# Kernel tuning notes

Measured on AMD Instinct MI355X. Metric: run time of the kernel, lower is better.

Reference implementation:

```python
import jax, jax.numpy as jnp
import numpy as np
import math

SEQ_LEN = 2048
EMB = 1024
HEAD = 64
BATCH = 8

def setup_inputs() -> dict:
    key = jax.random.key(0)
    k1, k2, k3, k4 = jax.random.split(key, 4)
    x = jax.random.normal(k1, (BATCH, SEQ_LEN, EMB), dtype=jnp.float32)
    # torch Linear(no bias): out = x @ W.T with W [out,in]; store as [in,out]
    s = 1.0 / math.sqrt(EMB)
    Wk = jax.random.uniform(k2, (EMB, HEAD), dtype=jnp.float32, minval=-s, maxval=s)
    Wq = jax.random.uniform(k3, (EMB, HEAD), dtype=jnp.float32, minval=-s, maxval=s)
    Wv = jax.random.uniform(k4, (EMB, HEAD), dtype=jnp.float32, minval=-s, maxval=s)
    return {"x": x, "Wk": Wk, "Wq": Wq, "Wv": Wv}

def reference(x, Wk, Wq, Wv):
    B, S, E = x.shape
    H = Wk.shape[1]
    k = x @ Wk  # [B,S,H]
    q = x @ Wq
    v = x @ Wv
    scores = jnp.einsum('bsh,bth->bst', q, k) / math.sqrt(H)
    causal = jnp.tril(jnp.ones((S, S), dtype=bool))
    scores = jnp.where(causal[None], scores, -jnp.inf)
    attn = jax.nn.softmax(scores, axis=-1)
    # dropout is identity in eval mode
    return jnp.einsum('bst,bth->bsh', attn, v)
```

## Files before the change

### kernel.cpp

```cpp
#include <hip/hip_runtime.h>
#include <hip/hip_bf16.h>

typedef __attribute__((ext_vector_type(8))) short short8;
typedef __attribute__((ext_vector_type(4))) short short4v;
typedef __attribute__((ext_vector_type(4))) float floatx4;

#define SEQ   2048
#define EMB   1024
#define HEAD  64
#define BATCH 8

__device__ __forceinline__ short f2bf(float f) {
    union { float f; unsigned u; } a; a.f = f;
    unsigned u = a.u;
    u = (u + 0x7FFFu + ((u >> 16) & 1u)) >> 16;
    return (short)u;
}

__device__ __forceinline__ void gld16(const void* g, void* l) {
    __builtin_amdgcn_global_load_lds(
        (const __attribute__((address_space(1))) unsigned int*)g,
        (__attribute__((address_space(3))) unsigned int*)l,
        16, 0, 0);
}

__global__ void wtrans_kernel(const float* __restrict__ Wk,
                              const float* __restrict__ Wq,
                              const float* __restrict__ Wv,
                              short* __restrict__ Wf) {
    int gid  = blockIdx.x * 256 + threadIdx.x;
    int lane = gid & 63;
    int fid  = gid >> 6;
    int chunk = fid & 31;
    int mnt  = fid >> 5;
    int mat  = mnt >> 2, nt = mnt & 3;
    const float* src = (mat == 0) ? Wq : (mat == 1) ? Wk : Wv;
    int n = lane & 15, quad = lane >> 4;
    int h = nt * 16 + n;
    short8 o8;
    #pragma unroll
    for (int j = 0; j < 8; ++j)
        o8[j] = f2bf(src[(chunk * 32 + quad * 8 + j) * 64 + h]);
    *(short8*)(Wf + (long)gid * 8) = o8;
}

__global__ __launch_bounds__(256, 1) void qkv_kernel(const float* __restrict__ x,
                                                     const short* __restrict__ Wf,
                                                     short* __restrict__ q,
                                                     short* __restrict__ k,
                                                     short* __restrict__ vt) {
    __shared__ short LW[2][12][4][64][8];
    const int wv   = threadIdx.x >> 6;
    const int lane = threadIdx.x & 63;
    const int l15  = lane & 15;
    const int quad = lane >> 4;
    const int row0 = blockIdx.x * 64 + wv * 16;

    floatx4 acc[12];
    #pragma unroll
    for (int f = 0; f < 12; ++f) acc[f] = (floatx4){0.f, 0.f, 0.f, 0.f};

    const float* xrow = x + (long)(row0 + l15) * EMB + quad * 8;

    #pragma unroll
    for (int i = 0; i < 12; ++i) {
        const int s = wv * 12 + i, mnt = s >> 2, c = s & 3;
        gld16(Wf + (long)(mnt * 32 + c) * 512 + lane * 8, &LW[0][mnt][c][0][0]);
    }
    __syncthreads();

    #pragma unroll 1
    for (int g = 0; g < 8; ++g) {
        const int bb = g & 1;
        const float* xg = xrow + g * 128;
        floatx4 xv[8];
        #pragma unroll
        for (int c = 0; c < 4; ++c) {
            xv[2 * c]     = *(const floatx4*)(xg + c * 32);
            xv[2 * c + 1] = *(const floatx4*)(xg + c * 32 + 4);
        }
        if (g < 7) {
            #pragma unroll
            for (int i = 0; i < 12; ++i) {
                const int s = wv * 12 + i, mnt = s >> 2, c = s & 3;
                gld16(Wf + (long)(mnt * 32 + (g + 1) * 4 + c) * 512 + lane * 8,
                      &LW[bb ^ 1][mnt][c][0][0]);
            }
        }
        #pragma unroll
        for (int c = 0; c < 4; ++c) {
            short8 a;
            #pragma unroll
            for (int i = 0; i < 4; ++i) {
                a[i]     = f2bf(xv[2 * c][i]);
                a[4 + i] = f2bf(xv[2 * c + 1][i]);
            }
            #pragma unroll
            for (int f = 0; f < 12; ++f) {
                short8 bf = *(const short8*)&LW[bb][f][c][lane][0];
                acc[f] = __builtin_amdgcn_mfma_f32_16x16x32_bf16(a, bf, acc[f], 0, 0, 0);
            }
        }
        __syncthreads();
    }

    const int bidx = row0 >> 11;
    const int srow = (row0 & (SEQ - 1)) + quad * 4;
    #pragma unroll
    for (int nt = 0; nt < 4; ++nt) {
        const int col = nt * 16 + l15;
        #pragma unroll
        for (int r = 0; r < 4; ++r) {
            long grow = (long)(row0 + quad * 4 + r);
            q[grow * HEAD + col] = f2bf(acc[nt][r]);
            k[grow * HEAD + col] = f2bf(acc[4 + nt][r]);
        }
        short4v vv;
        #pragma unroll
        for (int r = 0; r < 4; ++r) vv[r] = f2bf(acc[8 + nt][r]);
        *(short4v*)(vt + ((long)bidx * HEAD + col) * SEQ + srow) = vv;
    }
}

__global__ __launch_bounds__(256, 2) void attn_kernel(const short* __restrict__ q,
                                                      const short* __restrict__ k,
                                                      const short* __restrict__ vt,
                                                      float* __restrict__ out) {
    __shared__ short KV[2][16][64][8];
    __shared__ short Plds[4][16][40];
    __shared__ float oT[2][2][16][64];
    __shared__ float lT[2][2][16];

    const int wv   = threadIdx.x >> 6;
    const int lane = threadIdx.x & 63;
    const int l15  = lane & 15;
    const int quad = lane >> 4;
    const int rg   = wv & 1;
    const int kh   = wv >> 1;
    const int b    = blockIdx.x & 7;
    const int p    = blockIdx.x >> 3;
    const int t2   = 63 - p;
    const int s1   = p * 32, s2 = t2 * 32;
    const int nch1 = (p >> 1) + 1;
    const int nch2 = (t2 >> 1) + 1;

    const short* kbase = k  + (long)b * SEQ * HEAD;
    const short* vbase = vt + (long)b * HEAD * SEQ;

    const short* q1p = q + ((long)b * SEQ + s1 + rg * 16 + l15) * HEAD + quad * 8;
    const short* q2p = q + ((long)b * SEQ + s2 + rg * 16 + l15) * HEAD + quad * 8;
    short8 q1f0 = *(const short8*)(q1p), q1f1 = *(const short8*)(q1p + 32);
    short8 q2f0 = *(const short8*)(q2p), q2f1 = *(const short8*)(q2p + 32);

    floatx4 o1[4], o2[4];
    #pragma unroll
    for (int nh = 0; nh < 4; ++nh) {
        o1[nh] = (floatx4){0.f, 0.f, 0.f, 0.f};
        o2[nh] = (floatx4){0.f, 0.f, 0.f, 0.f};
    }
    float l1[4] = {0.f, 0.f, 0.f, 0.f};
    float l2[4] = {0.f, 0.f, 0.f, 0.f};

    auto stage = [&](int ch, int bb) {
        const int j0 = ch * 64;
        #pragma unroll
        for (int i = 0; i < 2; ++i) {
            const int fid = wv + i * 4;
            const int ntg = fid >> 1, ks = fid & 1;
            gld16(kbase + (long)(j0 + ntg * 16 + l15) * HEAD + ks * 32 + quad * 8,
                  &KV[bb][fid][0][0]);
        }
        #pragma unroll
        for (int i = 0; i < 2; ++i) {
            const int fid = wv + i * 4;
            const int kh2 = fid >> 2, nth = fid & 3;
            gld16(vbase + (long)(nth * 16 + l15) * SEQ + j0 + kh2 * 32 + quad * 8,
                  &KV[bb][8 + fid][0][0]);
        }
    };

    stage(0, 0);
    __syncthreads();

    #pragma unroll 1
    for (int ch = 0; ch < nch2; ++ch) {
        const int bb = ch & 1;
        if (ch + 1 < nch2) stage(ch + 1, bb ^ 1);
        const int j0 = ch * 64;

        short8 kf[2][2], vf[4];
        #pragma unroll
        for (int nt = 0; nt < 2; ++nt)
            #pragma unroll
            for (int ks = 0; ks < 2; ++ks)
                kf[nt][ks] = *(const short8*)&KV[bb][(kh * 2 + nt) * 2 + ks][lane][0];
        #pragma unroll
        for (int nh = 0; nh < 4; ++nh)
            vf[nh] = *(const short8*)&KV[bb][8 + kh * 4 + nh][lane][0];

        {
            floatx4 sa[2];
            sa[0] = (floatx4){0.f, 0.f, 0.f, 0.f};
            sa[1] = (floatx4){0.f, 0.f, 0.f, 0.f};
            #pragma unroll
            for (int nt = 0; nt < 2; ++nt) {
                sa[nt] = __builtin_amdgcn_mfma_f32_16x16x32_bf16(q2f0, kf[nt][0], sa[nt], 0, 0, 0);
                sa[nt] = __builtin_amdgcn_mfma_f32_16x16x32_bf16(q2f1, kf[nt][1], sa[nt], 0, 0, 0);
            }
            #pragma unroll
            for (int r = 0; r < 4; ++r) {
                const int sq = s2 + rg * 16 + quad * 4 + r;
                #pragma unroll
                for (int nt = 0; nt < 2; ++nt) {
                    const int sk = j0 + kh * 32 + nt * 16 + l15;
                    float pv = (sk > sq) ? 0.f : __expf(sa[nt][r] * 0.125f - 16.f);
                    sa[nt][r] = pv;
                    l2[r] += pv;
                }
            }
            #pragma unroll
            for (int nt = 0; nt < 2; ++nt)
                #pragma unroll
                for (int r = 0; r < 4; ++r)
                    Plds[wv][quad * 4 + r][nt * 16 + l15] = f2bf(sa[nt][r]);
            short8 pf = *(const short8*)(&Plds[wv][l15][quad * 8]);
            #pragma unroll
            for (int nh = 0; nh < 4; ++nh)
                o2[nh] = __builtin_amdgcn_mfma_f32_16x16x32_bf16(pf, vf[nh], o2[nh], 0, 0, 0);
        }

        if (ch < nch1) {
            floatx4 sa[2];
            sa[0] = (floatx4){0.f, 0.f, 0.f, 0.f};
            sa[1] = (floatx4){0.f, 0.f, 0.f, 0.f};
            #pragma unroll
            for (int nt = 0; nt < 2; ++nt) {
                sa[nt] = __builtin_amdgcn_mfma_f32_16x16x32_bf16(q1f0, kf[nt][0], sa[nt], 0, 0, 0);
                sa[nt] = __builtin_amdgcn_mfma_f32_16x16x32_bf16(q1f1, kf[nt][1], sa[nt], 0, 0, 0);
            }
            #pragma unroll
            for (int r = 0; r < 4; ++r) {
                const int sq = s1 + rg * 16 + quad * 4 + r;
                #pragma unroll
                for (int nt = 0; nt < 2; ++nt) {
                    const int sk = j0 + kh * 32 + nt * 16 + l15;
                    float pv = (sk > sq) ? 0.f : __expf(sa[nt][r] * 0.125f - 16.f);
                    sa[nt][r] = pv;
                    l1[r] += pv;
                }
            }
            #pragma unroll
            for (int nt = 0; nt < 2; ++nt)
                #pragma unroll
                for (int r = 0; r < 4; ++r)
                    Plds[wv][quad * 4 + r][nt * 16 + l15] = f2bf(sa[nt][r]);
            short8 pf = *(const short8*)(&Plds[wv][l15][quad * 8]);
            #pragma unroll
            for (int nh = 0; nh < 4; ++nh)
                o1[nh] = __builtin_amdgcn_mfma_f32_16x16x32_bf16(pf, vf[nh], o1[nh], 0, 0, 0);
        }
        __syncthreads();
    }

    #pragma unroll
    for (int msk = 1; msk <= 8; msk <<= 1) {
        #pragma unroll
        for (int r = 0; r < 4; ++r) {
            l1[r] += __shfl_xor(l1[r], msk, 64);
            l2[r] += __shfl_xor(l2[r], msk, 64);
        }
    }

    if (kh == 1) {
        #pragma unroll
        for (int nh = 0; nh < 4; ++nh)
            #pragma unroll
            for (int r = 0; r < 4; ++r) {
                oT[0][rg][quad * 4 + r][nh * 16 + l15] = o1[nh][r];
                oT[1][rg][quad * 4 + r][nh * 16 + l15] = o2[nh][r];
            }
        if (l15 == 0) {
            #pragma unroll
            for (int r = 0; r < 4; ++r) {
                lT[0][rg][quad * 4 + r] = l1[r];
                lT[1][rg][quad * 4 + r] = l2[r];
            }
        }
    }
    __syncthreads();
    if (kh == 0) {
        #pragma unroll
        for (int r = 0; r < 4; ++r) {
            const int row = quad * 4 + r;
            const float inv1 = 1.f / (l1[r] + lT[0][rg][row]);
            const float inv2 = 1.f / (l2[r] + lT[1][rg][row]);
            #pragma unroll
            for (int nh = 0; nh < 4; ++nh) {
                const int col = nh * 16 + l15;
                out[((long)b * SEQ + s1 + rg * 16 + row) * HEAD + col] =
                    (o1[nh][r] + oT[0][rg][row][col]) * inv1;
                out[((long)b * SEQ + s2 + rg * 16 + row) * HEAD + col] =
                    (o2[nh][r] + oT[1][rg][row][col]) * inv2;
            }
        }
    }
}

extern "C" void kernel_launch(void* const* d_in, const int* in_sizes, int n_in,
                              void* d_out, int out_size, void* d_ws, size_t ws_size,
                              hipStream_t stream) {
    const float* x  = (const float*)d_in[0];
    const float* Wk = (const float*)d_in[1];
    const float* Wq = (const float*)d_in[2];
    const float* Wv = (const float*)d_in[3];
    float* out = (float*)d_out;

    short* Wf = (short*)d_ws;
    short* q  = Wf + 3 * HEAD * EMB;
    short* k  = q + (long)BATCH * SEQ * HEAD;
    short* vt = k + (long)BATCH * SEQ * HEAD;

    hipLaunchKernelGGL(wtrans_kernel, dim3(96), dim3(256), 0, stream, Wk, Wq, Wv, Wf);
    hipLaunchKernelGGL(qkv_kernel, dim3(BATCH * SEQ / 64), dim3(256), 0, stream, x, Wf, q, k, vt);
    hipLaunchKernelGGL(attn_kernel, dim3(BATCH * 32), dim3(256), 0, stream, q, k, vt, out);
}
```

Before: 158.4 us.

## Retile QKV projection waves to 32 rows by 6 column tiles, cheaper bf16 rounding

Each wave of the QKV projection now computes two 16-row tiles against half of the 12 weight column tiles, rather than one 16-row tile against all 12. This halves the LDS weight reads per MFMA because each B fragment is reused for two A fragments, at the cost of more x-register loads per wave. The float-to-bf16 conversion also switches from round-to-nearest-even to a simpler round-half-up, saving ALU work but changing rounding on ties. The epilogue and some variable names in the attention kernel are adjusted to match.

```diff
diff --git a/kernel.cpp b/kernel.cpp
--- a/kernel.cpp
+++ b/kernel.cpp
@@ -12,9 +12,19 @@
 
 __device__ __forceinline__ short f2bf(float f) {
     union { float f; unsigned u; } a; a.f = f;
-    unsigned u = a.u;
-    u = (u + 0x7FFFu + ((u >> 16) & 1u)) >> 16;
-    return (short)u;
+    return (short)((a.u + 0x8000u) >> 16);
+}
+
+__device__ __forceinline__ short8 pk8(floatx4 a, floatx4 b) {
+    short8 r;
+    #pragma unroll
+    for (int i = 0; i < 4; ++i) {
+        union { float f; unsigned u; } x1, x2;
+        x1.f = a[i]; x2.f = b[i];
+        r[i]     = (short)((x1.u + 0x8000u) >> 16);
+        r[4 + i] = (short)((x2.u + 0x8000u) >> 16);
+    }
+    return r;
 }
 
 __device__ __forceinline__ void gld16(const void* g, void* l) {
@@ -54,13 +64,16 @@
     const int lane = threadIdx.x & 63;
     const int l15  = lane & 15;
     const int quad = lane >> 4;
-    const int row0 = blockIdx.x * 64 + wv * 16;
+    const int rg   = wv >> 1;
+    const int nh   = wv & 1;
+    const int row0 = blockIdx.x * 64;
 
     floatx4 acc[12];
     #pragma unroll
     for (int f = 0; f < 12; ++f) acc[f] = (floatx4){0.f, 0.f, 0.f, 0.f};
 
-    const float* xrow = x + (long)(row0 + l15) * EMB + quad * 8;
+    const float* xr0 = x + (long)(row0 + rg * 32 + l15) * EMB + quad * 8;
+    const float* xr1 = xr0 + (long)16 * EMB;
 
     #pragma unroll
     for (int i = 0; i < 12; ++i) {
@@ -72,12 +85,15 @@
     #pragma unroll 1
     for (int g = 0; g < 8; ++g) {
         const int bb = g & 1;
-        const float* xg = xrow + g * 128;
-        floatx4 xv[8];
+        floatx4 xv[16];
         #pragma unroll
         for (int c = 0; c < 4; ++c) {
-            xv[2 * c]     = *(const floatx4*)(xg + c * 32);
-            xv[2 * c + 1] = *(const floatx4*)(xg + c * 32 + 4);
+            const float* p0 = xr0 + g * 128 + c * 32;
+            const float* p1 = xr1 + g * 128 + c * 32;
+            xv[4 * c + 0] = *(const floatx4*)(p0);
+            xv[4 * c + 1] = *(const floatx4*)(p0 + 4);
+            xv[4 * c + 2] = *(const floatx4*)(p1);
+            xv[4 * c + 3] = *(const floatx4*)(p1 + 4);
         }
         if (g < 7) {
             #pragma unroll
@@ -89,36 +105,44 @@
         }
         #pragma unroll
         for (int c = 0; c < 4; ++c) {
-            short8 a;
-            #pragma unroll
-            for (int i = 0; i < 4; ++i) {
-                a[i]     = f2bf(xv[2 * c][i]);
-                a[4 + i] = f2bf(xv[2 * c + 1][i]);
-            }
-            #pragma unroll
-            for (int f = 0; f < 12; ++f) {
-                short8 bf = *(const short8*)&LW[bb][f][c][lane][0];
-                acc[f] = __builtin_amdgcn_mfma_f32_16x16x32_bf16(a, bf, acc[f], 0, 0, 0);
+            short8 a0 = pk8(xv[4 * c + 0], xv[4 * c + 1]);
+            short8 a1 = pk8(xv[4 * c + 2], xv[4 * c + 3]);
+            #pragma unroll
+            for (int i = 0; i < 6; ++i) {
+                short8 bf = *(const short8*)&LW[bb][nh * 6 + i][c][lane][0];
+                acc[i]     = __builtin_amdgcn_mfma_f32_16x16x32_bf16(a0, bf, acc[i], 0, 0, 0);
+                acc[6 + i] = __builtin_amdgcn_mfma_f32_16x16x32_bf16(a1, bf, acc[6 + i], 0, 0, 0);
             }
         }
         __syncthreads();
     }
 
     const int bidx = row0 >> 11;
-    const int srow = (row0 & (SEQ - 1)) + quad * 4;
-    #pragma unroll
-    for (int nt = 0; nt < 4; ++nt) {
-        const int col = nt * 16 + l15;
-        #pragma unroll
-        for (int r = 0; r < 4; ++r) {
-            long grow = (long)(row0 + quad * 4 + r);
-            q[grow * HEAD + col] = f2bf(acc[nt][r]);
-            k[grow * HEAD + col] = f2bf(acc[4 + nt][r]);
-        }
-        short4v vv;
-        #pragma unroll
-        for (int r = 0; r < 4; ++r) vv[r] = f2bf(acc[8 + nt][r]);
-        *(short4v*)(vt + ((long)bidx * HEAD + col) * SEQ + srow) = vv;
+    #pragma unroll
+    for (int i = 0; i < 6; ++i) {
+        const int mnt = nh * 6 + i;
+        const int mat = mnt >> 2, ntl = mnt & 3;
+        const int col = ntl * 16 + l15;
+        #pragma unroll
+        for (int rt = 0; rt < 2; ++rt) {
+            const floatx4 av = acc[rt * 6 + i];
+            const long rbase = row0 + rg * 32 + rt * 16 + quad * 4;
+            if (mat == 0) {
+                #pragma unroll
+                for (int r = 0; r < 4; ++r)
+                    q[(rbase + r) * HEAD + col] = f2bf(av[r]);
+            } else if (mat == 1) {
+                #pragma unroll
+                for (int r = 0; r < 4; ++r)
+                    k[(rbase + r) * HEAD + col] = f2bf(av[r]);
+            } else {
+                short4v vv;
+                #pragma unroll
+                for (int r = 0; r < 4; ++r) vv[r] = f2bf(av[r]);
+                const int srow = (int)(rbase & (SEQ - 1));
+                *(short4v*)(vt + ((long)bidx * HEAD + col) * SEQ + srow) = vv;
+            }
+        }
     }
 }
 
@@ -154,9 +178,9 @@
 
     floatx4 o1[4], o2[4];
     #pragma unroll
-    for (int nh = 0; nh < 4; ++nh) {
-        o1[nh] = (floatx4){0.f, 0.f, 0.f, 0.f};
-        o2[nh] = (floatx4){0.f, 0.f, 0.f, 0.f};
+    for (int nhh = 0; nhh < 4; ++nhh) {
+        o1[nhh] = (floatx4){0.f, 0.f, 0.f, 0.f};
+        o2[nhh] = (floatx4){0.f, 0.f, 0.f, 0.f};
     }
     float l1[4] = {0.f, 0.f, 0.f, 0.f};
     float l2[4] = {0.f, 0.f, 0.f, 0.f};
@@ -195,8 +219,8 @@
             for (int ks = 0; ks < 2; ++ks)
                 kf[nt][ks] = *(const short8*)&KV[bb][(kh * 2 + nt) * 2 + ks][lane][0];
         #pragma unroll
-        for (int nh = 0; nh < 4; ++nh)
-            vf[nh] = *(const short8*)&KV[bb][8 + kh * 4 + nh][lane][0];
+        for (int nhh = 0; nhh < 4; ++nhh)
+            vf[nhh] = *(const short8*)&KV[bb][8 + kh * 4 + nhh][lane][0];
 
         {
             floatx4 sa[2];
@@ -225,8 +249,8 @@
                     Plds[wv][quad * 4 + r][nt * 16 + l15] = f2bf(sa[nt][r]);
             short8 pf = *(const short8*)(&Plds[wv][l15][quad * 8]);
             #pragma unroll
-            for (int nh = 0; nh < 4; ++nh)
-                o2[nh] = __builtin_amdgcn_mfma_f32_16x16x32_bf16(pf, vf[nh], o2[nh], 0, 0, 0);
+            for (int nhh = 0; nhh < 4; ++nhh)
+                o2[nhh] = __builtin_amdgcn_mfma_f32_16x16x32_bf16(pf, vf[nhh], o2[nhh], 0, 0, 0);
         }
 
         if (ch < nch1) {
@@ -256,8 +280,8 @@
                     Plds[wv][quad * 4 + r][nt * 16 + l15] = f2bf(sa[nt][r]);
             short8 pf = *(const short8*)(&Plds[wv][l15][quad * 8]);
             #pragma unroll
-            for (int nh = 0; nh < 4; ++nh)
-                o1[nh] = __builtin_amdgcn_mfma_f32_16x16x32_bf16(pf, vf[nh], o1[nh], 0, 0, 0);
+            for (int nhh = 0; nhh < 4; ++nhh)
+                o1[nhh] = __builtin_amdgcn_mfma_f32_16x16x32_bf16(pf, vf[nhh], o1[nhh], 0, 0, 0);
         }
         __syncthreads();
     }
@@ -273,11 +297,11 @@
 
     if (kh == 1) {
         #pragma unroll
-        for (int nh = 0; nh < 4; ++nh)
+        for (int nhh = 0; nhh < 4; ++nhh)
             #pragma unroll
             for (int r = 0; r < 4; ++r) {
-                oT[0][rg][quad * 4 + r][nh * 16 + l15] = o1[nh][r];
-                oT[1][rg][quad * 4 + r][nh * 16 + l15] = o2[nh][r];
+                oT[0][rg][quad * 4 + r][nhh * 16 + l15] = o1[nhh][r];
+                oT[1][rg][quad * 4 + r][nhh * 16 + l15] = o2[nhh][r];
             }
         if (l15 == 0) {
             #pragma unroll
@@ -295,12 +319,12 @@
             const float inv1 = 1.f / (l1[r] + lT[0][rg][row]);
             const float inv2 = 1.f / (l2[r] + lT[1][rg][row]);
             #pragma unroll
-            for (int nh = 0; nh < 4; ++nh) {
-                const int col = nh * 16 + l15;
+            for (int nhh = 0; nhh < 4; ++nhh) {
+                const int col = nhh * 16 + l15;
                 out[((long)b * SEQ + s1 + rg * 16 + row) * HEAD + col] =
-                    (o1[nh][r] + oT[0][rg][row][col]) * inv1;
+                    (o1[nhh][r] + oT[0][rg][row][col]) * inv1;
                 out[((long)b * SEQ + s2 + rg * 16 + row) * HEAD + col] =
-                    (o2[nh][r] + oT[1][rg][row][col]) * inv2;
+                    (o2[nhh][r] + oT[1][rg][row][col]) * inv2;
             }
         }
     }
```

New measurement: 153.1 us. 3.4% less time.
